# Optimization experiments

Measured on AMD Instinct MI355X. Metric: run time of the kernel, lower is better.

## Reference

```python
import jax, jax.numpy as jnp
import numpy as np

T, B, X, H, Z = 28, 16384, 28, 100, 16
EPS = 1e-10


def setup_inputs() -> dict:
    key = jax.random.key(0)
    ks = jax.random.split(key, 32)
    s = 0.1  # weight scale to keep activations sane
    d = {
        'x': jax.random.uniform(ks[0], (T, B, X), jnp.float32),
        'eps': jax.random.normal(ks[1], (T, B, Z), jnp.float32),
        'Wpx': jax.random.normal(ks[2], (H, X)) * s, 'bpx': jnp.zeros((H,)),
        'Wpz': jax.random.normal(ks[3], (H, Z)) * s, 'bpz': jnp.zeros((H,)),
        'Wp1': jax.random.normal(ks[4], (H, H)) * s, 'bp1': jnp.zeros((H,)),
        'Wp_mu': jax.random.normal(ks[5], (Z, H)) * s, 'bp_mu': jnp.zeros((Z,)),
        'Wp_sig': jax.random.normal(ks[6], (Z, H)) * s, 'bp_sig': jnp.zeros((Z,)),
        'We1': jax.random.normal(ks[7], (H, 2 * H)) * s, 'be1': jnp.zeros((H,)),
        'We_mu': jax.random.normal(ks[8], (Z, H)) * s, 'be_mu': jnp.zeros((Z,)),
        'We_sig': jax.random.normal(ks[9], (Z, H)) * s, 'be_sig': jnp.zeros((Z,)),
        'Wd1': jax.random.normal(ks[10], (H, 2 * H)) * s, 'bd1': jnp.zeros((H,)),
        'Wd2': jax.random.normal(ks[11], (H, H)) * s, 'bd2': jnp.zeros((H,)),
        'Wd3': jax.random.normal(ks[12], (X, H)) * s, 'bd3': jnp.zeros((X,)),
        'Wih': jax.random.normal(ks[13], (3 * H, 2 * H)) * s, 'Whh': jax.random.normal(ks[14], (3 * H, H)) * s,
        'bih': jnp.zeros((3 * H,)), 'bhh': jnp.zeros((3 * H,)),
    }
    return {k: v.astype(jnp.float32) for k, v in d.items()}


def _lin(a, W, b):
    return a @ W.T + b


def reference(x, eps, Wpx, bpx, Wpz, bpz, Wp1, bp1, Wp_mu, bp_mu, Wp_sig, bp_sig,
              We1, be1, We_mu, be_mu, We_sig, be_sig, Wd1, bd1, Wd2, bd2, Wd3, bd3,
              Wih, Whh, bih, bhh):
    def step(h, inp):
        xt, et = inp  # [B,X], [B,Z]
        px = jax.nn.relu(_lin(xt, Wpx, bpx))  # phi_x
        # encoder q(z|x,h)
        he = jax.nn.relu(_lin(jnp.concatenate([px, h], -1), We1, be1))
        enc_mu = _lin(he, We_mu, be_mu)
        enc_sig = jax.nn.softplus(_lin(he, We_sig, be_sig))
        # prior p(z|h)
        hp = jax.nn.relu(_lin(h, Wp1, bp1))
        pr_mu = _lin(hp, Wp_mu, bp_mu)
        pr_sig = jax.nn.softplus(_lin(hp, Wp_sig, bp_sig))
        # reparameterize (torch code uses sqrt(scale) -- treat scale as var)
        z = enc_mu + jnp.sqrt(enc_sig) * et
        pz = jax.nn.relu(_lin(z, Wpz, bpz))  # phi_z
        # decoder p(x|z,h)
        hd = jax.nn.relu(_lin(jnp.concatenate([pz, h], -1), Wd1, bd1))
        hd = jax.nn.relu(_lin(hd, Wd2, bd2))
        probs = jax.nn.sigmoid(_lin(hd, Wd3, bd3))
        # GRUCell(input=[pz, px], h)
        gi = jnp.concatenate([pz, px], -1) @ Wih.T + bih
        gh = h @ Whh.T + bhh
        ir, iu, in_ = jnp.split(gi, 3, -1)
        hr, hu, hn = jnp.split(gh, 3, -1)
        r = jax.nn.sigmoid(ir + hr)
        u = jax.nn.sigmoid(iu + hu)
        n = jnp.tanh(in_ + r * hn)
        h_next = (1.0 - u) * n + u * h
        # KL(enc || prior)
        ps = pr_sig + EPS
        kl = 0.5 * (2 * jnp.log(ps) - 2 * jnp.log(enc_sig)
                    + (enc_sig ** 2 + (enc_mu - pr_mu) ** 2) / ps ** 2 - 1.0)
        kl = kl.sum(1).mean()
        # Bernoulli NLL
        nll = -(xt * jnp.log(probs + EPS) + (1.0 - xt) * jnp.log(1.0 - probs + EPS))
        nll = nll.sum(1).mean()
        return h_next, (kl, nll)

    h0 = jnp.zeros((x.shape[1], H), x.dtype)
    _, (kls, nlls) = jax.lax.scan(step, h0, (x, eps))
    return kls.sum(), nlls.sum()
```

## Files before the change

### kernel.cpp

```cpp
#include <hip/hip_runtime.h>
#include <math.h>

#define DEVFN __device__ __forceinline__

namespace {

typedef __bf16 bf16x8 __attribute__((ext_vector_type(8)));
typedef float  f32x4  __attribute__((ext_vector_type(4)));

constexpr int T = 28, B = 16384, X = 28, H = 100, Z = 16;
constexpr int ROWS = 16;
constexpr int NTH  = 128;
constexpr int ST   = 104;
constexpr int HBUF = ROWS*ST + 24;
constexpr int XST  = 40;
constexpr float KEPS = 1e-10f;

constexpr int FB_PX   = 0;
constexpr int FB_HE   = 7;
constexpr int FB_EMU  = 63;
constexpr int FB_ESIG = 67;
constexpr int FB_HP   = 71;
constexpr int FB_PMU  = 99;
constexpr int FB_PSIG = 103;
constexpr int FB_PZ   = 107;
constexpr int FB_HD1  = 114;
constexpr int FB_HD2  = 170;
constexpr int FB_PRB  = 198;
constexpr int FB_GIR  = 206;
constexpr int FB_GIU  = 262;
constexpr int FB_GIN  = 318;
constexpr int FB_GHR  = 374;
constexpr int FB_GHU  = 402;
constexpr int FB_GHN  = 430;
constexpr int NFRAG   = 458;

struct Params {
  const float *x,*eps,*Wpx,*bpx,*Wpz,*bpz,*Wp1,*bp1,*Wp_mu,*bp_mu,*Wp_sig,*bp_sig,
              *We1,*be1,*We_mu,*be_mu,*We_sig,*be_sig,*Wd1,*bd1,*Wd2,*bd2,*Wd3,*bd3,
              *Wih,*Whh,*bih,*bhh;
  float *out;
};

DEVFN float frcp(float x){ return __builtin_amdgcn_rcpf(x); }
DEVFN float fsigmoid(float v){ return frcp(1.f + __expf(-v)); }
DEVFN float ftanh(float v){
  float t = __expf(-2.f*fabsf(v));
  float r = (1.f - t) * frcp(1.f + t);
  return copysignf(r, v);
}
DEVFN float fsoftplus(float v){
  float sp = (v > 15.f) ? v : __logf(1.f + __expf(v));
  return fmaxf(sp, 1e-6f);
}

DEVFN f32x4 MFMA(bf16x8 a, bf16x8 b, f32x4 c){
  return __builtin_amdgcn_mfma_f32_16x16x32_bf16(a, b, c, 0, 0, 0);
}

__global__ void prep_kernel(Params P, __bf16* FRW)
{
  const int f = blockIdx.x, l = threadIdx.x;
  const int bases[18] = {FB_PX,FB_HE,FB_EMU,FB_ESIG,FB_HP,FB_PMU,FB_PSIG,FB_PZ,FB_HD1,
                         FB_HD2,FB_PRB,FB_GIR,FB_GIU,FB_GIN,FB_GHR,FB_GHU,FB_GHN,NFRAG};
  int li = 0;
  while (f >= bases[li+1]) ++li;

  const float* W; const float* Bv; int KT, N, roff, wstr, vK, mode;
  switch (li) {
    case 0:  W=P.Wpx;    Bv=P.bpx;    KT=1; N=100; roff=0;   wstr=28;  vK=28;  mode=0; break;
    case 1:  W=P.We1;    Bv=P.be1;    KT=8; N=100; roff=0;   wstr=200; vK=100; mode=1; break;
    case 2:  W=P.We_mu;  Bv=P.be_mu;  KT=4; N=16;  roff=0;   wstr=100; vK=100; mode=0; break;
    case 3:  W=P.We_sig; Bv=P.be_sig; KT=4; N=16;  roff=0;   wstr=100; vK=100; mode=0; break;
    case 4:  W=P.Wp1;    Bv=P.bp1;    KT=4; N=100; roff=0;   wstr=100; vK=100; mode=0; break;
    case 5:  W=P.Wp_mu;  Bv=P.bp_mu;  KT=4; N=16;  roff=0;   wstr=100; vK=100; mode=0; break;
    case 6:  W=P.Wp_sig; Bv=P.bp_sig; KT=4; N=16;  roff=0;   wstr=100; vK=100; mode=0; break;
    case 7:  W=P.Wpz;    Bv=P.bpz;    KT=1; N=100; roff=0;   wstr=16;  vK=16;  mode=0; break;
    case 8:  W=P.Wd1;    Bv=P.bd1;    KT=8; N=100; roff=0;   wstr=200; vK=100; mode=1; break;
    case 9:  W=P.Wd2;    Bv=P.bd2;    KT=4; N=100; roff=0;   wstr=100; vK=100; mode=0; break;
    case 10: W=P.Wd3;    Bv=P.bd3;    KT=4; N=28;  roff=0;   wstr=100; vK=100; mode=0; break;
    case 11: W=P.Wih;    Bv=P.bih;    KT=8; N=100; roff=0;   wstr=200; vK=100; mode=1; break;
    case 12: W=P.Wih;    Bv=P.bih;    KT=8; N=100; roff=100; wstr=200; vK=100; mode=1; break;
    case 13: W=P.Wih;    Bv=P.bih;    KT=8; N=100; roff=200; wstr=200; vK=100; mode=1; break;
    case 14: W=P.Whh;    Bv=P.bhh;    KT=4; N=100; roff=0;   wstr=100; vK=100; mode=0; break;
    case 15: W=P.Whh;    Bv=P.bhh;    KT=4; N=100; roff=100; wstr=100; vK=100; mode=0; break;
    default: W=P.Whh;    Bv=P.bhh;    KT=4; N=100; roff=200; wstr=100; vK=100; mode=0; break;
  }
  const int idx = f - bases[li];
  const int nt = idx / KT, kc = idx % KT;
  const int n  = nt*16 + (l & 15);

  bf16x8 v;
  #pragma unroll
  for (int j = 0; j < 8; ++j) {
    int kk  = (mode ? (kc & 3) : kc)*32 + ((l >> 4)*8) + j;
    float w = 0.f;
    if (n < N) {
      if (mode == 0) {
        if (kk < vK)       w = W[(size_t)(roff + n)*wstr + kk];
        else if (kk == vK) w = Bv[roff + n];
      } else {
        int col = (kc < 4 ? 0 : 100) + kk;
        if (kk < 100)                    w = W[(size_t)(roff + n)*wstr + col];
        else if (kc < 4 && kk == 100)    w = Bv[roff + n];
      }
    }
    v[j] = (__bf16)w;
  }
  *((bf16x8*)FRW + (size_t)f*64 + l) = v;
}

template<int NC>
DEVFN void load_afrags(bf16x8 (&af)[NC], const __bf16* A, int stride, int lane)
{
  const __bf16* p = A + (size_t)(lane & 15)*stride + ((lane >> 4)*8);
  #pragma unroll
  for (int kc = 0; kc < NC; ++kc) af[kc] = *(const bf16x8*)(p + kc*32);
}

template<int KT, int NA>
DEVFN void layerH(const bf16x8 (&af)[NA], const bf16x8* FRbase, __bf16* dst, int sw, int lane)
{
  for (int nt = sw; nt < 7; nt += 2) {
    f32x4 acc = {0.f,0.f,0.f,0.f};
    const bf16x8* wf = FRbase + (size_t)nt*KT*64 + lane;
    #pragma unroll
    for (int kc = 0; kc < KT; ++kc) acc = MFMA(af[kc], wf[kc*64], acc);
    const int col = nt*16 + (lane & 15);
    if (col < H) {
      const int rbase = (lane >> 4)*4;
      #pragma unroll
      for (int r = 0; r < 4; ++r)
        dst[(size_t)(rbase + r)*ST + col] = (__bf16)fmaxf(acc[r], 0.f);
    }
  }
}

DEVFN void layerHcat(const bf16x8 (&a0)[4], const bf16x8 (&a1)[4], const bf16x8* FRbase,
                     __bf16* dst, int sw, int lane)
{
  for (int nt = sw; nt < 7; nt += 2) {
    f32x4 acc = {0.f,0.f,0.f,0.f};
    const bf16x8* wf = FRbase + (size_t)nt*8*64 + lane;
    #pragma unroll
    for (int kc = 0; kc < 4; ++kc) acc = MFMA(a0[kc], wf[kc*64], acc);
    #pragma unroll
    for (int kc = 0; kc < 4; ++kc) acc = MFMA(a1[kc], wf[(4+kc)*64], acc);
    const int col = nt*16 + (lane & 15);
    if (col < H) {
      const int rbase = (lane >> 4)*4;
      #pragma unroll
      for (int r = 0; r < 4; ++r)
        dst[(size_t)(rbase + r)*ST + col] = (__bf16)fmaxf(acc[r], 0.f);
    }
  }
}

template<int KT>
DEVFN f32x4 head4(const bf16x8 (&af)[KT], const bf16x8* FRbase, int lane)
{
  f32x4 acc = {0.f,0.f,0.f,0.f};
  #pragma unroll
  for (int kc = 0; kc < KT; ++kc) acc = MFMA(af[kc], FRbase[kc*64 + lane], acc);
  return acc;
}

__global__ __launch_bounds__(NTH, 2) void vrnn_kernel(Params P, const __bf16* FRW)
{
  __shared__ alignas(16) __bf16 sPX[HBUF];
  __shared__ alignas(16) __bf16 sPZ[HBUF];
  __shared__ alignas(16) __bf16 sA [HBUF];
  __shared__ alignas(16) __bf16 sB [HBUF];
  __shared__ alignas(16) __bf16 sH [HBUF];
  __shared__ alignas(16) __bf16 sZ [ROWS*XST];
  __shared__ float sred[4];

  const bf16x8* FR = (const bf16x8*)FRW;
  const int tid  = threadIdx.x;
  const int lane = tid & 63;
  const int wv   = tid >> 6;
  const int gr0  = blockIdx.x * ROWS;

  for (int i = tid; i < HBUF; i += NTH) {
    sPX[i]=(__bf16)0.f; sPZ[i]=(__bf16)0.f; sA[i]=(__bf16)0.f; sB[i]=(__bf16)0.f; sH[i]=(__bf16)0.f;
  }
  for (int i = tid; i < ROWS*XST; i += NTH) sZ[i]=(__bf16)0.f;
  __syncthreads();
  if (tid < ROWS) {
    sPX[tid*ST+100]=(__bf16)1.f; sPZ[tid*ST+100]=(__bf16)1.f; sA[tid*ST+100]=(__bf16)1.f;
    sB [tid*ST+100]=(__bf16)1.f; sH [tid*ST+100]=(__bf16)1.f; sZ[tid*XST+16]=(__bf16)1.f;
  }
  __syncthreads();

  float kl = 0.f, nll = 0.f;

  for (int t = 0; t < T; ++t) {
    {
      const int m = lane & 15, quad = lane >> 4;
      const float* xr = P.x + ((size_t)t*B + gr0 + m)*X + quad*8;
      float4 fa = *(const float4*)xr;
      float4 fb = make_float4(0.f,0.f,0.f,0.f);
      if (quad < 3) fb = *(const float4*)(xr + 4);
      bf16x8 ax;
      ax[0]=(__bf16)fa.x; ax[1]=(__bf16)fa.y; ax[2]=(__bf16)fa.z; ax[3]=(__bf16)fa.w;
      ax[4]=(__bf16)fb.x; ax[5]=(__bf16)fb.y; ax[6]=(__bf16)fb.z; ax[7]=(__bf16)fb.w;
      if (quad == 3) ax[4] = (__bf16)1.f;
      bf16x8 axA[1] = {ax};
      layerH<1,1>(axA, FR + (size_t)FB_PX*64, sPX, wv, lane);
      bf16x8 ah[4]; load_afrags(ah, sH, ST, lane);
      layerH<4,4>(ah, FR + (size_t)FB_HP*64, sB, wv ^ 1, lane);
    }
    __syncthreads();

    {
      bf16x8 a0[4]; load_afrags(a0, sPX, ST, lane);
      bf16x8 a1[4]; load_afrags(a1, sH,  ST, lane);
      layerHcat(a0, a1, FR + (size_t)FB_HE*64, sA, wv, lane);
    }
    __syncthreads();

    {
      bf16x8 a1[4]; load_afrags(a1, sA, ST, lane);
      bf16x8 a2[4]; load_afrags(a2, sB, ST, lane);
      f32x4 emu = head4(a1, FR + (size_t)FB_EMU*64,  lane);
      f32x4 esg = head4(a1, FR + (size_t)FB_ESIG*64, lane);
      f32x4 pmu = head4(a2, FR + (size_t)FB_PMU*64,  lane);
      f32x4 psg = head4(a2, FR + (size_t)FB_PSIG*64, lane);
      const int zi = lane & 15;
      const int rbase = (lane >> 4)*4;
      #pragma unroll
      for (int r = 0; r < 4; ++r) {
        float em = emu[r];
        float es = fsoftplus(esg[r]);
        float ev = P.eps[((size_t)t*B + gr0 + rbase + r)*Z + zi];
        sZ[(rbase + r)*XST + zi] = (__bf16)(em + __builtin_amdgcn_sqrtf(es)*ev);
        if ((r >> 1) == wv) {
          float ps = fsoftplus(psg[r]) + KEPS;
          float dm = em - pmu[r];
          float rps = frcp(ps);
          kl += 0.5f*(2.f*__logf(ps*frcp(es)) + (es*es + dm*dm)*(rps*rps) - 1.f);
        }
      }
    }

    {
      bf16x8 az[1]; load_afrags(az, sZ, XST, lane);
      layerH<1,1>(az, FR + (size_t)FB_PZ*64, sPZ, wv ^ 1, lane);
    }
    __syncthreads();

    {
      bf16x8 apz[4]; load_afrags(apz, sPZ, ST, lane);
      bf16x8 ah [4]; load_afrags(ah,  sH,  ST, lane);
      bf16x8 apx[4]; load_afrags(apx, sPX, ST, lane);
      __syncthreads();

      layerHcat(apz, ah, FR + (size_t)FB_HD1*64, sA, wv, lane);

      for (int c = (wv ^ 1); c < 7; c += 2) {
        f32x4 gr={0.f,0.f,0.f,0.f}, gu={0.f,0.f,0.f,0.f}, gn={0.f,0.f,0.f,0.f};
        f32x4 hr={0.f,0.f,0.f,0.f}, hu={0.f,0.f,0.f,0.f}, hn={0.f,0.f,0.f,0.f};
        const bf16x8* wr = FR + (size_t)(FB_GIR + c*8)*64 + lane;
        const bf16x8* wu = FR + (size_t)(FB_GIU + c*8)*64 + lane;
        const bf16x8* wn = FR + (size_t)(FB_GIN + c*8)*64 + lane;
        #pragma unroll
        for (int kc = 0; kc < 4; ++kc) {
          bf16x8 a = apz[kc];
          gr = MFMA(a, wr[kc*64], gr); gu = MFMA(a, wu[kc*64], gu); gn = MFMA(a, wn[kc*64], gn);
        }
        #pragma unroll
        for (int kc = 0; kc < 4; ++kc) {
          bf16x8 a = apx[kc];
          gr = MFMA(a, wr[(4+kc)*64], gr); gu = MFMA(a, wu[(4+kc)*64], gu); gn = MFMA(a, wn[(4+kc)*64], gn);
        }
        const bf16x8* vr = FR + (size_t)(FB_GHR + c*4)*64 + lane;
        const bf16x8* vu = FR + (size_t)(FB_GHU + c*4)*64 + lane;
        const bf16x8* vn = FR + (size_t)(FB_GHN + c*4)*64 + lane;
        #pragma unroll
        for (int kc = 0; kc < 4; ++kc) {
          bf16x8 a = ah[kc];
          hr = MFMA(a, vr[kc*64], hr); hu = MFMA(a, vu[kc*64], hu); hn = MFMA(a, vn[kc*64], hn);
        }
        const int n = c*16 + (lane & 15);
        if (n < H) {
          const int rbase = (lane >> 4)*4;
          #pragma unroll
          for (int r = 0; r < 4; ++r) {
            float rr = fsigmoid(gr[r] + hr[r]);
            float uu = fsigmoid(gu[r] + hu[r]);
            float nn = ftanh(gn[r] + rr*hn[r]);
            float ho = (float)sH[(size_t)(rbase+r)*ST + n];
            sH[(size_t)(rbase+r)*ST + n] = (__bf16)((1.f-uu)*nn + uu*ho);
          }
        }
      }
    }
    __syncthreads();

    {
      bf16x8 af[4]; load_afrags(af, sA, ST, lane);
      layerH<4,4>(af, FR + (size_t)FB_HD2*64, sB, wv, lane);
    }
    __syncthreads();

    {
      bf16x8 af[4]; load_afrags(af, sB, ST, lane);
      f32x4 acc = head4(af, FR + (size_t)(FB_PRB + wv*4)*64, lane);
      const int n = wv*16 + (lane & 15);
      if (n < X) {
        const int rbase = (lane >> 4)*4;
        #pragma unroll
        for (int r = 0; r < 4; ++r) {
          float v  = acc[r];
          float xv = P.x[((size_t)t*B + gr0 + rbase + r)*X + n];
          nll += fmaxf(-v, 0.f) + __logf(1.f + __expf(-fabsf(v))) + (1.f - xv)*v;
        }
      }
    }
    __syncthreads();
  }

  for (int off = 32; off > 0; off >>= 1) {
    kl  += __shfl_down(kl,  off);
    nll += __shfl_down(nll, off);
  }
  if (lane == 0) { sred[wv] = kl; sred[2 + wv] = nll; }
  __syncthreads();
  if (tid == 0) {
    atomicAdd(&P.out[0], (sred[0] + sred[1]) * (1.f/(float)B));
    atomicAdd(&P.out[1], (sred[2] + sred[3]) * (1.f/(float)B));
  }
}

}

extern "C" void kernel_launch(void* const* d_in, const int* in_sizes, int n_in,
                              void* d_out, int out_size, void* d_ws, size_t ws_size,
                              hipStream_t stream)
{
  Params p;
  const float* const* f = (const float* const*)d_in;
  p.x=f[0];    p.eps=f[1];
  p.Wpx=f[2];  p.bpx=f[3];   p.Wpz=f[4];   p.bpz=f[5];
  p.Wp1=f[6];  p.bp1=f[7];   p.Wp_mu=f[8]; p.bp_mu=f[9];
  p.Wp_sig=f[10]; p.bp_sig=f[11];
  p.We1=f[12]; p.be1=f[13];  p.We_mu=f[14]; p.be_mu=f[15];
  p.We_sig=f[16]; p.be_sig=f[17];
  p.Wd1=f[18]; p.bd1=f[19];  p.Wd2=f[20];  p.bd2=f[21];
  p.Wd3=f[22]; p.bd3=f[23];
  p.Wih=f[24]; p.Whh=f[25];  p.bih=f[26];  p.bhh=f[27];
  p.out = (float*)d_out;

  hipMemsetAsync(d_out, 0, 2*sizeof(float), stream);
  prep_kernel<<<dim3(NFRAG), dim3(64), 0, stream>>>(p, (__bf16*)d_ws);
  vrnn_kernel<<<dim3(B/ROWS), dim3(NTH), 0, stream>>>(p, (const __bf16*)d_ws);
}
```

Baseline: 691.3 us.

## Split per-block work across four waves instead of two

Doubles the block size to 256 threads, so four wavefronts share each 16-row tile. Every layer's column tiles, the GRU gate chunks, the KL and the output-head rows are now redistributed among four waves. Decoder layer 1 and the GRU are load-balanced by hand, with wave 3 taking the extra hd1 tiles. The aim is to cut the serial MFMA chain per wave within each recurrent step and shorten the per-step critical path. The cost is more barrier participants, lower per-wave utilisation and higher register-pressure constraints from launch_bounds(256,4).

Measured after the change: 1.314 ms. +90.1%, slower.

```diff
diff --git a/kernel.cpp b/kernel.cpp
--- a/kernel.cpp
+++ b/kernel.cpp
@@ -10,7 +10,7 @@
 
 constexpr int T = 28, B = 16384, X = 28, H = 100, Z = 16;
 constexpr int ROWS = 16;
-constexpr int NTH  = 128;
+constexpr int NTH  = 256;
 constexpr int ST   = 104;
 constexpr int HBUF = ROWS*ST + 24;
 constexpr int XST  = 40;
@@ -119,9 +119,9 @@
 }
 
 template<int KT, int NA>
-DEVFN void layerH(const bf16x8 (&af)[NA], const bf16x8* FRbase, __bf16* dst, int sw, int lane)
-{
-  for (int nt = sw; nt < 7; nt += 2) {
+DEVFN void layerH(const bf16x8 (&af)[NA], const bf16x8* FRbase, __bf16* dst, int sw, int step, int lane)
+{
+  for (int nt = sw; nt < 7; nt += step) {
     f32x4 acc = {0.f,0.f,0.f,0.f};
     const bf16x8* wf = FRbase + (size_t)nt*KT*64 + lane;
     #pragma unroll
@@ -136,24 +136,28 @@
   }
 }
 
+DEVFN void layerHcat1(const bf16x8 (&a0)[4], const bf16x8 (&a1)[4], const bf16x8* FRbase,
+                      __bf16* dst, int nt, int lane)
+{
+  f32x4 acc = {0.f,0.f,0.f,0.f};
+  const bf16x8* wf = FRbase + (size_t)nt*8*64 + lane;
+  #pragma unroll
+  for (int kc = 0; kc < 4; ++kc) acc = MFMA(a0[kc], wf[kc*64], acc);
+  #pragma unroll
+  for (int kc = 0; kc < 4; ++kc) acc = MFMA(a1[kc], wf[(4+kc)*64], acc);
+  const int col = nt*16 + (lane & 15);
+  if (col < H) {
+    const int rbase = (lane >> 4)*4;
+    #pragma unroll
+    for (int r = 0; r < 4; ++r)
+      dst[(size_t)(rbase + r)*ST + col] = (__bf16)fmaxf(acc[r], 0.f);
+  }
+}
+
 DEVFN void layerHcat(const bf16x8 (&a0)[4], const bf16x8 (&a1)[4], const bf16x8* FRbase,
-                     __bf16* dst, int sw, int lane)
-{
-  for (int nt = sw; nt < 7; nt += 2) {
-    f32x4 acc = {0.f,0.f,0.f,0.f};
-    const bf16x8* wf = FRbase + (size_t)nt*8*64 + lane;
-    #pragma unroll
-    for (int kc = 0; kc < 4; ++kc) acc = MFMA(a0[kc], wf[kc*64], acc);
-    #pragma unroll
-    for (int kc = 0; kc < 4; ++kc) acc = MFMA(a1[kc], wf[(4+kc)*64], acc);
-    const int col = nt*16 + (lane & 15);
-    if (col < H) {
-      const int rbase = (lane >> 4)*4;
-      #pragma unroll
-      for (int r = 0; r < 4; ++r)
-        dst[(size_t)(rbase + r)*ST + col] = (__bf16)fmaxf(acc[r], 0.f);
-    }
-  }
+                     __bf16* dst, int sw, int step, int lane)
+{
+  for (int nt = sw; nt < 7; nt += step) layerHcat1(a0, a1, FRbase, dst, nt, lane);
 }
 
 template<int KT>
@@ -165,7 +169,7 @@
   return acc;
 }
 
-__global__ __launch_bounds__(NTH, 2) void vrnn_kernel(Params P, const __bf16* FRW)
+__global__ __launch_bounds__(NTH, 4) void vrnn_kernel(Params P, const __bf16* FRW)
 {
   __shared__ alignas(16) __bf16 sPX[HBUF];
   __shared__ alignas(16) __bf16 sPZ[HBUF];
@@ -173,7 +177,7 @@
   __shared__ alignas(16) __bf16 sB [HBUF];
   __shared__ alignas(16) __bf16 sH [HBUF];
   __shared__ alignas(16) __bf16 sZ [ROWS*XST];
-  __shared__ float sred[4];
+  __shared__ float sred[8];
 
   const bf16x8* FR = (const bf16x8*)FRW;
   const int tid  = threadIdx.x;
@@ -206,16 +210,16 @@
       ax[4]=(__bf16)fb.x; ax[5]=(__bf16)fb.y; ax[6]=(__bf16)fb.z; ax[7]=(__bf16)fb.w;
       if (quad == 3) ax[4] = (__bf16)1.f;
       bf16x8 axA[1] = {ax};
-      layerH<1,1>(axA, FR + (size_t)FB_PX*64, sPX, wv, lane);
+      layerH<1,1>(axA, FR + (size_t)FB_PX*64, sPX, wv, 4, lane);
       bf16x8 ah[4]; load_afrags(ah, sH, ST, lane);
-      layerH<4,4>(ah, FR + (size_t)FB_HP*64, sB, wv ^ 1, lane);
+      layerH<4,4>(ah, FR + (size_t)FB_HP*64, sB, (wv + 1) & 3, 4, lane);
     }
     __syncthreads();
 
     {
       bf16x8 a0[4]; load_afrags(a0, sPX, ST, lane);
       bf16x8 a1[4]; load_afrags(a1, sH,  ST, lane);
-      layerHcat(a0, a1, FR + (size_t)FB_HE*64, sA, wv, lane);
+      layerHcat(a0, a1, FR + (size_t)FB_HE*64, sA, wv, 4, lane);
     }
     __syncthreads();
 
@@ -234,7 +238,7 @@
         float es = fsoftplus(esg[r]);
         float ev = P.eps[((size_t)t*B + gr0 + rbase + r)*Z + zi];
         sZ[(rbase + r)*XST + zi] = (__bf16)(em + __builtin_amdgcn_sqrtf(es)*ev);
-        if ((r >> 1) == wv) {
+        if (r == wv) {
           float ps = fsoftplus(psg[r]) + KEPS;
           float dm = em - pmu[r];
           float rps = frcp(ps);
@@ -245,7 +249,7 @@
 
     {
       bf16x8 az[1]; load_afrags(az, sZ, XST, lane);
-      layerH<1,1>(az, FR + (size_t)FB_PZ*64, sPZ, wv ^ 1, lane);
+      layerH<1,1>(az, FR + (size_t)FB_PZ*64, sPZ, wv, 4, lane);
     }
     __syncthreads();
 
@@ -255,9 +259,14 @@
       bf16x8 apx[4]; load_afrags(apx, sPX, ST, lane);
       __syncthreads();
 
-      layerHcat(apz, ah, FR + (size_t)FB_HD1*64, sA, wv, lane);
-
-      for (int c = (wv ^ 1); c < 7; c += 2) {
+      if (wv == 3) {
+        for (int nt = 0; nt < 7; nt += 2)
+          layerHcat1(apz, ah, FR + (size_t)FB_HD1*64, sA, nt, lane);
+      } else {
+        layerHcat1(apz, ah, FR + (size_t)FB_HD1*64, sA, 2*wv + 1, lane);
+      }
+
+      for (int c = wv; c < 7; c += 4) {
         f32x4 gr={0.f,0.f,0.f,0.f}, gu={0.f,0.f,0.f,0.f}, gn={0.f,0.f,0.f,0.f};
         f32x4 hr={0.f,0.f,0.f,0.f}, hu={0.f,0.f,0.f,0.f}, hn={0.f,0.f,0.f,0.f};
         const bf16x8* wr = FR + (size_t)(FB_GIR + c*8)*64 + lane;
@@ -299,18 +308,21 @@
 
     {
       bf16x8 af[4]; load_afrags(af, sA, ST, lane);
-      layerH<4,4>(af, FR + (size_t)FB_HD2*64, sB, wv, lane);
+      layerH<4,4>(af, FR + (size_t)FB_HD2*64, sB, wv, 4, lane);
     }
     __syncthreads();
 
     {
       bf16x8 af[4]; load_afrags(af, sB, ST, lane);
-      f32x4 acc = head4(af, FR + (size_t)(FB_PRB + wv*4)*64, lane);
-      const int n = wv*16 + (lane & 15);
+      const int pt = wv & 1;
+      const int rh = (wv >> 1) * 2;
+      f32x4 acc = head4(af, FR + (size_t)(FB_PRB + pt*4)*64, lane);
+      const int n = pt*16 + (lane & 15);
       if (n < X) {
         const int rbase = (lane >> 4)*4;
         #pragma unroll
-        for (int r = 0; r < 4; ++r) {
+        for (int rr = 0; rr < 2; ++rr) {
+          const int r = rh + rr;
           float v  = acc[r];
           float xv = P.x[((size_t)t*B + gr0 + rbase + r)*X + n];
           nll += fmaxf(-v, 0.f) + __logf(1.f + __expf(-fabsf(v))) + (1.f - xv)*v;
@@ -324,11 +336,11 @@
     kl  += __shfl_down(kl,  off);
     nll += __shfl_down(nll, off);
   }
-  if (lane == 0) { sred[wv] = kl; sred[2 + wv] = nll; }
+  if (lane == 0) { sred[wv] = kl; sred[4 + wv] = nll; }
   __syncthreads();
   if (tid == 0) {
-    atomicAdd(&P.out[0], (sred[0] + sred[1]) * (1.f/(float)B));
-    atomicAdd(&P.out[1], (sred[2] + sred[3]) * (1.f/(float)B));
+    atomicAdd(&P.out[0], (sred[0] + sred[1] + sred[2] + sred[3]) * (1.f/(float)B));
+    atomicAdd(&P.out[1], (sred[4] + sred[5] + sred[6] + sred[7]) * (1.f/(float)B));
   }
 }
 
```
